# Kernel optimization log

Hardware: AMD Instinct MI355X
Metric: run time of the kernel (lower is better)

The kernel has to match this reference:

```python
import jax, jax.numpy as jnp
import numpy as np

N = 50000      # nodes
E = 800000     # edges (before self loops)
F_IN = 128     # dataset.num_features
HID = 32       # hidden_channels (per GAT head)
HEADS = 4
C = 40         # dataset.num_classes
NEG_SLOPE = 0.2


def setup_inputs() -> dict:
    key = jax.random.key(0)
    ks = jax.random.split(key, 18)
    g = lambda k, shape, fan: jax.random.normal(k, shape, dtype=jnp.float32) / np.sqrt(fan)
    inp = {
        "x": jax.random.normal(ks[0], (N, F_IN), dtype=jnp.float32),
        "edge_index": jax.random.randint(ks[1], (2, E), 0, N, dtype=jnp.int64),
        # GAT layer 1: F_IN -> HEADS*HID
        "gat_W1": g(ks[2], (F_IN, HEADS * HID), F_IN),
        "gat_att_src1": g(ks[3], (HEADS, HID), HID),
        "gat_att_dst1": g(ks[4], (HEADS, HID), HID),
        "gat_b1": jnp.zeros((HEADS * HID,), jnp.float32),
        # GAT layer 2: HEADS*HID -> C, heads=1
        "gat_W2": g(ks[5], (HEADS * HID, C), HEADS * HID),
        "gat_att_src2": g(ks[6], (1, C), C),
        "gat_att_dst2": g(ks[7], (1, C), C),
        "gat_b2": jnp.zeros((C,), jnp.float32),
        # GCN layers
        "gcn_W1": g(ks[8], (F_IN, HID), F_IN),
        "gcn_b1": jnp.zeros((HID,), jnp.float32),
        "gcn_W2": g(ks[9], (HID, C), HID),
        "gcn_b2": jnp.zeros((C,), jnp.float32),
        # final linear: 2C -> C
        "lin_W": g(ks[10], (2 * C, C), 2 * C),
        "lin_b": jnp.zeros((C,), jnp.float32),
        "weight_c": jnp.float32(0.5),
        "weight_t": jnp.float32(0.5),
    }
    return inp


def _add_self_loops(src, dst, n):
    loop = jnp.arange(n, dtype=src.dtype)
    return jnp.concatenate([src, loop]), jnp.concatenate([dst, loop])


def _gat_conv(x, src, dst, n, W, att_src, att_dst, b, heads, out_dim):
    # h: [n, heads, out_dim]
    h = (x @ W).reshape(n, heads, out_dim)
    a_s = jnp.einsum('nhd,hd->nh', h, att_src)   # source-side attention logit
    a_d = jnp.einsum('nhd,hd->nh', h, att_dst)   # target-side attention logit
    e = jax.nn.leaky_relu(a_s[src] + a_d[dst], NEG_SLOPE)  # [E', heads]
    # softmax over incoming edges of each target node (self loops guarantee >=1 edge)
    m = jax.ops.segment_max(e, dst, num_segments=n)
    ex = jnp.exp(e - m[dst])
    s = jax.ops.segment_sum(ex, dst, num_segments=n)
    alpha = ex / s[dst]                          # [E', heads]
    out = jax.ops.segment_sum(h[src] * alpha[..., None], dst, num_segments=n)
    return out.reshape(n, heads * out_dim) + b


def _gcn_conv(x, src, dst, n, W, b):
    h = x @ W
    deg = jax.ops.segment_sum(jnp.ones(src.shape, h.dtype), dst, num_segments=n)
    norm = jax.lax.rsqrt(deg)                    # deg >= 1 (self loops)
    coef = (norm[src] * norm[dst])[:, None]
    return jax.ops.segment_sum(h[src] * coef, dst, num_segments=n) + b


def reference(x, edge_index, gat_W1, gat_att_src1, gat_att_dst1, gat_b1,
              gat_W2, gat_att_src2, gat_att_dst2, gat_b2,
              gcn_W1, gcn_b1, gcn_W2, gcn_b2, lin_W, lin_b,
              weight_c, weight_t):
    n = x.shape[0]
    src, dst = _add_self_loops(edge_index[0], edge_index[1], n)
    # GAT branch (dropout is identity at inference)
    x_gat = _gat_conv(x, src, dst, n, gat_W1, gat_att_src1, gat_att_dst1,
                      gat_b1, HEADS, HID)
    x_gat = jax.nn.elu(x_gat)
    x_gat = _gat_conv(x_gat, src, dst, n, gat_W2, gat_att_src2, gat_att_dst2,
                      gat_b2, 1, C)
    # GCN branch
    x_gcn = jax.nn.relu(_gcn_conv(x, src, dst, n, gcn_W1, gcn_b1))
    x_gcn = _gcn_conv(x_gcn, src, dst, n, gcn_W2, gcn_b2)
    # weighted feature concat + linear head
    cat = jnp.concatenate([x_gcn * weight_c, x_gat * weight_t], axis=1)  # [n, 2C]
    return cat @ lin_W + lin_b
```

## Files before the change

kernel.cpp:

```cpp
#include <hip/hip_runtime.h>
#include <math.h>

#define F_IN   128
#define HIDC   32
#define NHEAD  4
#define CDIM   40
#define NEG_SLOPE 0.2f
#define BCAP   4096
#define OVCAP  16384
#define SCHUNK 4096

typedef __attribute__((ext_vector_type(8))) short bf16x8;
typedef __attribute__((ext_vector_type(4))) float f32x4;

__device__ __forceinline__ float leakyf(float x) { return x > 0.f ? x : NEG_SLOPE * x; }

__device__ __forceinline__ float wred_max(float v) {
#pragma unroll
    for (int o = 32; o > 0; o >>= 1) v = fmaxf(v, __shfl_xor(v, o, 64));
    return v;
}
__device__ __forceinline__ float wred_sum(float v) {
#pragma unroll
    for (int o = 32; o > 0; o >>= 1) v += __shfl_xor(v, o, 64);
    return v;
}
__device__ __forceinline__ float sel4(float4 v, int h) {
    return (h == 0) ? v.x : (h == 1) ? v.y : (h == 2) ? v.z : v.w;
}
__device__ __forceinline__ unsigned pack2_bf16(float a, float b) {
    unsigned ua = __float_as_uint(a);
    unsigned ub = __float_as_uint(b);
    ua = (ua + 0x7FFFu + ((ua >> 16) & 1u)) >> 16;
    ub = (ub + 0x7FFFu + ((ub >> 16) & 1u)) >> 16;
    return ua | (ub << 16);
}
__device__ __forceinline__ float2 unpack2_bf16(unsigned p) {
    return make_float2(__uint_as_float(p << 16), __uint_as_float(p & 0xFFFF0000u));
}

__global__ void wb_prep_kernel(const float* __restrict__ Wg, const float* __restrict__ Wc,
                               uint4* __restrict__ wbf)
{
    int b = blockIdx.x;
    int lane = threadIdx.x;
    int nt = b >> 2, ks = b & 3;
    int c = nt * 16 + (lane & 15);
    int k0 = ks * 32 + (lane >> 4) * 8;
    unsigned u[4];
#pragma unroll
    for (int jj = 0; jj < 4; ++jj) {
        int k = k0 + 2 * jj;
        float a0 = (c < 128) ? Wg[(size_t)k * 128 + c] : Wc[(size_t)k * 32 + (c - 128)];
        float a1 = (c < 128) ? Wg[(size_t)(k + 1) * 128 + c] : Wc[(size_t)(k + 1) * 32 + (c - 128)];
        u[jj] = pack2_bf16(a0, a1);
    }
    wbf[(size_t)b * 64 + lane] = make_uint4(u[0], u[1], u[2], u[3]);
}

__global__ __launch_bounds__(256) void gemm1_mfma_kernel(
    const float* __restrict__ X, const uint4* __restrict__ wbf,
    const float* __restrict__ aw_s, const float* __restrict__ aw_d,
    unsigned* __restrict__ h1b, unsigned* __restrict__ g1b,
    float* __restrict__ as1, float* __restrict__ ad1, int n)
{
    __shared__ float Ct[64][164];
    __shared__ float sw[128], dw[128];
    const int tid = threadIdx.x;
    const int w = tid >> 6, lane = tid & 63;
    const int m = lane & 15, q = lane >> 4;
    const int node0 = blockIdx.x * 64;
    if (tid < 128) { sw[tid] = aw_s[tid]; dw[tid] = aw_d[tid]; }

    f32x4 acc[10];
#pragma unroll
    for (int t = 0; t < 10; ++t) acc[t] = (f32x4){0.f, 0.f, 0.f, 0.f};

    const int row = node0 + w * 16 + m;
    const bool rv = row < n;
#pragma unroll
    for (int ks = 0; ks < 4; ++ks) {
        uint4 pa = make_uint4(0u, 0u, 0u, 0u);
        if (rv) {
            const float* xr = X + (size_t)row * 128 + ks * 32 + q * 8;
            float4 a0 = *(const float4*)xr;
            float4 a1 = *(const float4*)(xr + 4);
            pa = make_uint4(pack2_bf16(a0.x, a0.y), pack2_bf16(a0.z, a0.w),
                            pack2_bf16(a1.x, a1.y), pack2_bf16(a1.z, a1.w));
        }
        bf16x8 af = *(bf16x8*)&pa;
#pragma unroll
        for (int nt = 0; nt < 10; ++nt) {
            uint4 pb = wbf[(size_t)(nt * 4 + ks) * 64 + lane];
            bf16x8 bfv = *(bf16x8*)&pb;
            acc[nt] = __builtin_amdgcn_mfma_f32_16x16x32_bf16(af, bfv, acc[nt], 0, 0, 0);
        }
    }
#pragma unroll
    for (int nt = 0; nt < 10; ++nt)
#pragma unroll
        for (int r = 0; r < 4; ++r)
            Ct[w * 16 + q * 4 + r][nt * 16 + m] = acc[nt][r];
    __syncthreads();

    for (int i = tid; i < 64 * 64; i += 256) {
        int nd = i >> 6, u = i & 63;
        int gn = node0 + nd;
        if (gn < n)
            h1b[(size_t)gn * 64 + u] = pack2_bf16(Ct[nd][2 * u], Ct[nd][2 * u + 1]);
    }
    for (int i = tid; i < 64 * 16; i += 256) {
        int nd = i >> 4, u = i & 15;
        int gn = node0 + nd;
        if (gn < n)
            g1b[(size_t)gn * 16 + u] = pack2_bf16(Ct[nd][128 + 2 * u], Ct[nd][128 + 2 * u + 1]);
    }
    {
        int nd = tid >> 2, h = tid & 3;
        int gn = node0 + nd;
        if (gn < n) {
            float s = 0.f, d = 0.f;
#pragma unroll
            for (int k = 0; k < HIDC; ++k) {
                float v = Ct[nd][h * HIDC + k];
                s = fmaf(v, sw[h * HIDC + k], s);
                d = fmaf(v, dw[h * HIDC + k], d);
            }
            as1[(size_t)gn * 4 + h] = s;
            ad1[(size_t)gn * 4 + h] = d;
        }
    }
}

template<int K, int OUTC, int BN, int BK, int OSTRIDE = OUTC>
__global__ __launch_bounds__((OUTC / 4) * (BN / 4)) void gemm_tile(
    const float* __restrict__ X, const float* __restrict__ W,
    const float* __restrict__ bias, float* __restrict__ Y, int n)
{
    constexpr int CG = OUTC / 4;
    constexpr int NG = BN / 4;
    constexpr int NT = CG * NG;
    __shared__ float Xs[BK][BN + 4];
    __shared__ float Ws[BK][OUTC];
    const int tid = threadIdx.x;
    const int cg = tid % CG, ng = tid / CG;
    const int node0 = blockIdx.x * BN;
    float acc[4][4] = {};

    for (int kb = 0; kb < K; kb += BK) {
        for (int idx = tid; idx < BN * (BK / 4); idx += NT) {
            int nd = idx / (BK / 4);
            int kq = idx % (BK / 4);
            int gnode = node0 + nd;
            float4 v = (gnode < n) ? *(const float4*)&X[(size_t)gnode * K + kb + kq * 4]
                                   : make_float4(0.f, 0.f, 0.f, 0.f);
            Xs[kq * 4 + 0][nd] = v.x;
            Xs[kq * 4 + 1][nd] = v.y;
            Xs[kq * 4 + 2][nd] = v.z;
            Xs[kq * 4 + 3][nd] = v.w;
        }
        for (int idx = tid; idx < BK * CG; idx += NT) {
            int kk = idx / CG;
            int cq = idx % CG;
            *(float4*)&Ws[kk][cq * 4] = *(const float4*)&W[(size_t)(kb + kk) * OUTC + cq * 4];
        }
        __syncthreads();
#pragma unroll
        for (int k = 0; k < BK; ++k) {
            float4 xv = *(const float4*)&Xs[k][ng * 4];
            float4 wv = *(const float4*)&Ws[k][cg * 4];
            float xa[4] = {xv.x, xv.y, xv.z, xv.w};
            float wa[4] = {wv.x, wv.y, wv.z, wv.w};
#pragma unroll
            for (int j = 0; j < 4; ++j)
#pragma unroll
                for (int c = 0; c < 4; ++c)
                    acc[j][c] = fmaf(xa[j], wa[c], acc[j][c]);
        }
        __syncthreads();
    }

    float4 bv = make_float4(0.f, 0.f, 0.f, 0.f);
    if (bias) bv = *(const float4*)&bias[cg * 4];
#pragma unroll
    for (int j = 0; j < 4; ++j) {
        int gnode = node0 + ng * 4 + j;
        if (gnode < n) {
            float4 o = make_float4(acc[j][0] + bv.x, acc[j][1] + bv.y,
                                   acc[j][2] + bv.z, acc[j][3] + bv.w);
            *(float4*)&Y[(size_t)gnode * OSTRIDE + cg * 4] = o;
        }
    }
}

template<int K, int OUTC, int BN, int BK, int OSTRIDE_U, int OFF_U>
__global__ __launch_bounds__((OUTC / 4) * (BN / 4)) void gemm_tile_b(
    const float* __restrict__ X, const float* __restrict__ W,
    unsigned* __restrict__ Yb, int n)
{
    constexpr int CG = OUTC / 4;
    constexpr int NG = BN / 4;
    constexpr int NT = CG * NG;
    __shared__ float Xs[BK][BN + 4];
    __shared__ float Ws[BK][OUTC];
    const int tid = threadIdx.x;
    const int cg = tid % CG, ng = tid / CG;
    const int node0 = blockIdx.x * BN;
    float acc[4][4] = {};

    for (int kb = 0; kb < K; kb += BK) {
        for (int idx = tid; idx < BN * (BK / 4); idx += NT) {
            int nd = idx / (BK / 4);
            int kq = idx % (BK / 4);
            int gnode = node0 + nd;
            float4 v = (gnode < n) ? *(const float4*)&X[(size_t)gnode * K + kb + kq * 4]
                                   : make_float4(0.f, 0.f, 0.f, 0.f);
            Xs[kq * 4 + 0][nd] = v.x;
            Xs[kq * 4 + 1][nd] = v.y;
            Xs[kq * 4 + 2][nd] = v.z;
            Xs[kq * 4 + 3][nd] = v.w;
        }
        for (int idx = tid; idx < BK * CG; idx += NT) {
            int kk = idx / CG;
            int cq = idx % CG;
            *(float4*)&Ws[kk][cq * 4] = *(const float4*)&W[(size_t)(kb + kk) * OUTC + cq * 4];
        }
        __syncthreads();
#pragma unroll
        for (int k = 0; k < BK; ++k) {
            float4 xv = *(const float4*)&Xs[k][ng * 4];
            float4 wv = *(const float4*)&Ws[k][cg * 4];
            float xa[4] = {xv.x, xv.y, xv.z, xv.w};
            float wa[4] = {wv.x, wv.y, wv.z, wv.w};
#pragma unroll
            for (int j = 0; j < 4; ++j)
#pragma unroll
                for (int c = 0; c < 4; ++c)
                    acc[j][c] = fmaf(xa[j], wa[c], acc[j][c]);
        }
        __syncthreads();
    }

#pragma unroll
    for (int j = 0; j < 4; ++j) {
        int gnode = node0 + ng * 4 + j;
        if (gnode < n) {
            uint2 pb = make_uint2(pack2_bf16(acc[j][0], acc[j][1]),
                                  pack2_bf16(acc[j][2], acc[j][3]));
            *(uint2*)&Yb[(size_t)gnode * OSTRIDE_U + OFF_U + cg * 2] = pb;
        }
    }
}

template<int K, int OUTC, int BN, int BK, int OSTRIDE_U, int OFF_U>
__global__ __launch_bounds__((OUTC / 4) * (BN / 4)) void gemm_tile_bb(
    const unsigned* __restrict__ Xb, const float* __restrict__ W,
    unsigned* __restrict__ Yb, int n)
{
    constexpr int CG = OUTC / 4;
    constexpr int NG = BN / 4;
    constexpr int NT = CG * NG;
    __shared__ float Xs[BK][BN + 4];
    __shared__ float Ws[BK][OUTC];
    const int tid = threadIdx.x;
    const int cg = tid % CG, ng = tid / CG;
    const int node0 = blockIdx.x * BN;
    float acc[4][4] = {};

    for (int kb = 0; kb < K; kb += BK) {
        for (int idx = tid; idx < BN * (BK / 8); idx += NT) {
            int nd = idx / (BK / 8);
            int kq = idx % (BK / 8);
            int gnode = node0 + nd;
            uint4 v = (gnode < n) ? *(const uint4*)&Xb[(size_t)gnode * (K / 2) + kb / 2 + kq * 4]
                                  : make_uint4(0u, 0u, 0u, 0u);
            float2 a = unpack2_bf16(v.x), b = unpack2_bf16(v.y);
            float2 c = unpack2_bf16(v.z), d = unpack2_bf16(v.w);
            Xs[kq * 8 + 0][nd] = a.x; Xs[kq * 8 + 1][nd] = a.y;
            Xs[kq * 8 + 2][nd] = b.x; Xs[kq * 8 + 3][nd] = b.y;
            Xs[kq * 8 + 4][nd] = c.x; Xs[kq * 8 + 5][nd] = c.y;
            Xs[kq * 8 + 6][nd] = d.x; Xs[kq * 8 + 7][nd] = d.y;
        }
        for (int idx = tid; idx < BK * CG; idx += NT) {
            int kk = idx / CG;
            int cq = idx % CG;
            *(float4*)&Ws[kk][cq * 4] = *(const float4*)&W[(size_t)(kb + kk) * OUTC + cq * 4];
        }
        __syncthreads();
#pragma unroll
        for (int k = 0; k < BK; ++k) {
            float4 xv = *(const float4*)&Xs[k][ng * 4];
            float4 wv = *(const float4*)&Ws[k][cg * 4];
            float xa[4] = {xv.x, xv.y, xv.z, xv.w};
            float wa[4] = {wv.x, wv.y, wv.z, wv.w};
#pragma unroll
            for (int j = 0; j < 4; ++j)
#pragma unroll
                for (int c = 0; c < 4; ++c)
                    acc[j][c] = fmaf(xa[j], wa[c], acc[j][c]);
        }
        __syncthreads();
    }

#pragma unroll
    for (int j = 0; j < 4; ++j) {
        int gnode = node0 + ng * 4 + j;
        if (gnode < n) {
            uint2 pb = make_uint2(pack2_bf16(acc[j][0], acc[j][1]),
                                  pack2_bf16(acc[j][2], acc[j][3]));
            *(uint2*)&Yb[(size_t)gnode * OSTRIDE_U + OFF_U + cg * 2] = pb;
        }
    }
}

__global__ __launch_bounds__(256) void bucket_scatter_kernel(
    const int* __restrict__ src, const int* __restrict__ dst,
    unsigned* __restrict__ bcnt, unsigned* __restrict__ bpair,
    unsigned* __restrict__ ovf_cnt, uint2* __restrict__ ovf, int e, int nbuck)
{
    __shared__ unsigned hist[512];
    __shared__ unsigned base[512];
    const int t = threadIdx.x;
    const int lo = blockIdx.x * SCHUNK;
    const int hi = min(lo + SCHUNK, e);
    for (int i = t; i < nbuck; i += 256) hist[i] = 0;
    __syncthreads();
    for (int i = lo + t; i < hi; i += 256)
        atomicAdd(&hist[((unsigned)dst[i]) >> 7], 1u);
    __syncthreads();
    for (int i = t; i < nbuck; i += 256) {
        unsigned c = hist[i];
        base[i] = c ? atomicAdd(&bcnt[i], c) : 0u;
        hist[i] = 0;
    }
    __syncthreads();
    for (int i = lo + t; i < hi; i += 256) {
        unsigned s = (unsigned)src[i], d = (unsigned)dst[i];
        unsigned b = d >> 7;
        unsigned pos = base[b] + atomicAdd(&hist[b], 1u);
        if (pos < BCAP) bpair[(size_t)b * BCAP + pos] = s | ((d & 127u) << 16);
        else {
            unsigned o = atomicAdd(ovf_cnt, 1u);
            if (o < OVCAP) ovf[o] = make_uint2(s, d);
        }
    }
}

__global__ __launch_bounds__(256) void bucket_count_kernel(
    const unsigned* __restrict__ bcnt, const unsigned* __restrict__ bpair,
    const unsigned* __restrict__ ovf_cnt, const uint2* __restrict__ ovf,
    unsigned* __restrict__ counts, int n)
{
    __shared__ unsigned lc[128];
    const int b = blockIdx.x, base = b << 7;
    if (threadIdx.x < 128) lc[threadIdx.x] = 0;
    __syncthreads();
    unsigned bc = bcnt[b];
    int cnt = (int)(bc < BCAP ? bc : BCAP);
    for (int k = threadIdx.x; k < cnt; k += 256)
        atomicAdd(&lc[bpair[(size_t)b * BCAP + k] >> 16], 1u);
    unsigned oc_u = *ovf_cnt;
    int oc = (int)(oc_u < OVCAP ? oc_u : OVCAP);
    for (int k = threadIdx.x; k < oc; k += 256) {
        uint2 pp = ovf[k];
        if ((int)(pp.y >> 7) == b) atomicAdd(&lc[pp.y & 127u], 1u);
    }
    __syncthreads();
    int i = base + threadIdx.x;
    if (threadIdx.x < 128 && i < n) counts[i] = lc[threadIdx.x];
}

__global__ __launch_bounds__(256) void scan_reduce_kernel(const unsigned* __restrict__ counts,
                                                          unsigned* __restrict__ partials, int n)
{
    __shared__ unsigned sm[256];
    int t = threadIdx.x;
    int i = blockIdx.x * 256 + t;
    unsigned v = (i < n) ? counts[i] : 0u;
    sm[t] = v;
    __syncthreads();
#pragma unroll
    for (int off = 128; off > 0; off >>= 1) {
        if (t < off) sm[t] += sm[t + off];
        __syncthreads();
    }
    if (t == 0) partials[blockIdx.x] = sm[0];
}

__global__ __launch_bounds__(256) void scan_partials_kernel(unsigned* __restrict__ partials,
                                                            unsigned* __restrict__ rs, int nb, int n)
{
    __shared__ unsigned sm[256];
    int t = threadIdx.x;
    unsigned v = (t < nb) ? partials[t] : 0u;
    sm[t] = v;
    __syncthreads();
#pragma unroll
    for (int off = 1; off < 256; off <<= 1) {
        unsigned u = (t >= off) ? sm[t - off] : 0u;
        __syncthreads();
        sm[t] += u;
        __syncthreads();
    }
    if (t < nb) partials[t] = sm[t] - v;
    if (t == 255) rs[n] = sm[255];
}

__global__ __launch_bounds__(256) void scan_write_kernel(const unsigned* __restrict__ counts,
                                                         const unsigned* __restrict__ partials,
                                                         unsigned* __restrict__ rs,
                                                         float* __restrict__ nrm, int n)
{
    __shared__ unsigned sm[256];
    int t = threadIdx.x;
    int i = blockIdx.x * 256 + t;
    unsigned c = (i < n) ? counts[i] : 0u;
    sm[t] = c;
    __syncthreads();
#pragma unroll
    for (int off = 1; off < 256; off <<= 1) {
        unsigned u = (t >= off) ? sm[t - off] : 0u;
        __syncthreads();
        sm[t] += u;
        __syncthreads();
    }
    if (i < n) {
        rs[i] = partials[blockIdx.x] + sm[t] - c;
        nrm[i] = rsqrtf((float)(c + 1u));
    }
}

__global__ __launch_bounds__(256) void bucket_place_kernel(
    const unsigned* __restrict__ bcnt, const unsigned* __restrict__ bpair,
    const unsigned* __restrict__ rs, unsigned* __restrict__ csr_src,
    unsigned* __restrict__ cursor, int n)
{
    __shared__ unsigned lc[128];
    __shared__ unsigned rbase[128];
    const int b = blockIdx.x, base = b << 7;
    if (threadIdx.x < 128) {
        lc[threadIdx.x] = 0;
        int i = base + threadIdx.x;
        rbase[threadIdx.x] = (i < n) ? rs[i] : 0u;
    }
    __syncthreads();
    unsigned bc = bcnt[b];
    int cnt = (int)(bc < BCAP ? bc : BCAP);
    for (int k = threadIdx.x; k < cnt; k += 256) {
        unsigned v = bpair[(size_t)b * BCAP + k];
        unsigned ld = v >> 16;
        unsigned r = atomicAdd(&lc[ld], 1u);
        csr_src[rbase[ld] + r] = v & 0xFFFFu;
    }
    __syncthreads();
    int i = base + threadIdx.x;
    if (threadIdx.x < 128 && i < n) cursor[i] = rbase[threadIdx.x] + lc[threadIdx.x];
}

__global__ void overflow_fill_kernel(const unsigned* __restrict__ ovf_cnt,
                                     const uint2* __restrict__ ovf,
                                     unsigned* __restrict__ cursor,
                                     unsigned* __restrict__ csr_src)
{
    unsigned oc_u = *ovf_cnt;
    int oc = (int)(oc_u < OVCAP ? oc_u : OVCAP);
    for (int k = threadIdx.x; k < oc; k += 256) {
        uint2 pp = ovf[k];
        unsigned pos = atomicAdd(&cursor[pp.y], 1u);
        csr_src[pos] = pp.x;
    }
}

__global__ void logits2_kernel(const unsigned* __restrict__ hg_b, const float* __restrict__ aw_s,
                               const float* __restrict__ aw_d, float* __restrict__ as2,
                               float* __restrict__ ad2, int n)
{
    __shared__ float sw[CDIM], dw[CDIM];
    if (threadIdx.x < CDIM) { sw[threadIdx.x] = aw_s[threadIdx.x]; dw[threadIdx.x] = aw_d[threadIdx.x]; }
    __syncthreads();
    int i = blockIdx.x * 256 + threadIdx.x;
    if (i >= n) return;
    const unsigned* row = hg_b + (size_t)i * 40;
    float s = 0.f, d = 0.f;
#pragma unroll
    for (int k = 0; k < 20; ++k) {
        float2 v = unpack2_bf16(row[k]);
        s = fmaf(v.x, sw[2 * k], s);     s = fmaf(v.y, sw[2 * k + 1], s);
        d = fmaf(v.x, dw[2 * k], d);     d = fmaf(v.y, dw[2 * k + 1], d);
    }
    as2[i] = s; ad2[i] = d;
}

#define CAP1 96
__global__ __launch_bounds__(256) void gat_agg1_kernel(
    const unsigned* __restrict__ h1b,
    const float* __restrict__ as1, const float* __restrict__ ad1,
    const unsigned* __restrict__ rs, const unsigned* __restrict__ csr_src,
    const float* __restrict__ b1, unsigned* __restrict__ xgb, int n)
{
    __shared__ unsigned sidx[4][CAP1];
    __shared__ float    w4[4][CAP1][4];
    const int wid = threadIdx.x >> 6;
    const int lane = threadIdx.x & 63;
    const int i = blockIdx.x * 4 + wid;
    if (i >= n) return;
    const unsigned beg = rs[i];
    const int deg = (int)(rs[i + 1] - beg);
    const float4* as1v = (const float4*)as1;
    float4 av = as1v[i];
    float4 dv = ((const float4*)ad1)[i];
    float4 es = make_float4(leakyf(av.x + dv.x), leakyf(av.y + dv.y),
                            leakyf(av.z + dv.z), leakyf(av.w + dv.w));
    float m0 = es.x, m1 = es.y, m2 = es.z, m3 = es.w;
    for (int k = lane; k < deg; k += 64) {
        unsigned s = csr_src[beg + k];
        float4 a = as1v[s];
        float e0 = leakyf(a.x + dv.x), e1 = leakyf(a.y + dv.y);
        float e2 = leakyf(a.z + dv.z), e3 = leakyf(a.w + dv.w);
        if (k < CAP1) {
            sidx[wid][k] = s;
            w4[wid][k][0] = e0; w4[wid][k][1] = e1;
            w4[wid][k][2] = e2; w4[wid][k][3] = e3;
        }
        m0 = fmaxf(m0, e0); m1 = fmaxf(m1, e1);
        m2 = fmaxf(m2, e2); m3 = fmaxf(m3, e3);
    }
    m0 = wred_max(m0); m1 = wred_max(m1); m2 = wred_max(m2); m3 = wred_max(m3);
    float s0 = 0.f, s1 = 0.f, s2 = 0.f, s3 = 0.f;
    if (lane == 0) {
        s0 = __expf(es.x - m0); s1 = __expf(es.y - m1);
        s2 = __expf(es.z - m2); s3 = __expf(es.w - m3);
    }
    const int dc = deg < CAP1 ? deg : CAP1;
    for (int k = lane; k < dc; k += 64) {
        float w0 = __expf(w4[wid][k][0] - m0); w4[wid][k][0] = w0; s0 += w0;
        float w1 = __expf(w4[wid][k][1] - m1); w4[wid][k][1] = w1; s1 += w1;
        float w2 = __expf(w4[wid][k][2] - m2); w4[wid][k][2] = w2; s2 += w2;
        float w3 = __expf(w4[wid][k][3] - m3); w4[wid][k][3] = w3; s3 += w3;
    }
    for (int k = CAP1 + lane; k < deg; k += 64) {
        unsigned s = csr_src[beg + k];
        float4 a = as1v[s];
        s0 += __expf(leakyf(a.x + dv.x) - m0);
        s1 += __expf(leakyf(a.y + dv.y) - m1);
        s2 += __expf(leakyf(a.z + dv.z) - m2);
        s3 += __expf(leakyf(a.w + dv.w) - m3);
    }
    s0 = wred_sum(s0); s1 = wred_sum(s1); s2 = wred_sum(s2); s3 = wred_sum(s3);
    __threadfence_block();
    const int h = lane >> 4;
    const float mh   = sel4(make_float4(m0, m1, m2, m3), h);
    const float advh = sel4(dv, h);
    const float ssh  = sel4(make_float4(s0, s1, s2, s3), h);
    const float wself = __expf(sel4(es, h) - mh);
    float2 hv = unpack2_bf16(h1b[(size_t)i * 64 + lane]);
    float2 acc = make_float2(hv.x * wself, hv.y * wself);
    auto edge = [&](int j, unsigned& s, float& w) {
        if (j < CAP1) { s = sidx[wid][j]; w = w4[wid][j][h]; }
        else {
            s = csr_src[beg + j];
            float4 a = as1v[s];
            w = __expf(leakyf(sel4(a, h) + advh) - mh);
        }
    };
    int j = 0;
    for (; j + 4 <= deg; j += 4) {
        unsigned sa, sb, sc, sd; float wa, wb, wc, wd;
        edge(j, sa, wa); edge(j + 1, sb, wb); edge(j + 2, sc, wc); edge(j + 3, sd, wd);
        float2 va = unpack2_bf16(h1b[(size_t)sa * 64 + lane]);
        float2 vb = unpack2_bf16(h1b[(size_t)sb * 64 + lane]);
        float2 vc = unpack2_bf16(h1b[(size_t)sc * 64 + lane]);
        float2 vd = unpack2_bf16(h1b[(size_t)sd * 64 + lane]);
        acc.x = fmaf(va.x, wa, acc.x); acc.y = fmaf(va.y, wa, acc.y);
        acc.x = fmaf(vb.x, wb, acc.x); acc.y = fmaf(vb.y, wb, acc.y);
        acc.x = fmaf(vc.x, wc, acc.x); acc.y = fmaf(vc.y, wc, acc.y);
        acc.x = fmaf(vd.x, wd, acc.x); acc.y = fmaf(vd.y, wd, acc.y);
    }
    for (; j < deg; ++j) {
        unsigned s; float w; edge(j, s, w);
        float2 v = unpack2_bf16(h1b[(size_t)s * 64 + lane]);
        acc.x = fmaf(v.x, w, acc.x); acc.y = fmaf(v.y, w, acc.y);
    }
    float inv = 1.f / ssh;
    int c0 = 2 * lane;
    float o0 = acc.x * inv + b1[c0];
    float o1 = acc.y * inv + b1[c0 + 1];
    o0 = o0 > 0.f ? o0 : __expf(o0) - 1.f;
    o1 = o1 > 0.f ? o1 : __expf(o1) - 1.f;
    xgb[(size_t)i * 64 + lane] = pack2_bf16(o0, o1);
}

#define CAP2 128
__global__ __launch_bounds__(256) void agg2_fused_kernel(
    const unsigned* __restrict__ hg_b, const float* __restrict__ as2,
    const float* __restrict__ ad2, const float* __restrict__ nrm,
    const unsigned* __restrict__ rs, const unsigned* __restrict__ csr_src,
    const float* __restrict__ gat_b2, const float* __restrict__ gcn_b2,
    const float* __restrict__ wc_p, const float* __restrict__ wt_p,
    float* __restrict__ cat, int n)
{
    __shared__ unsigned sidx[4][CAP2];
    __shared__ float    wgt[4][CAP2];
    __shared__ float    cf [4][CAP2];
    const int wid = threadIdx.x >> 6;
    const int lane = threadIdx.x & 63;
    const int i = blockIdx.x * 4 + wid;
    if (i >= n) return;
    const unsigned beg = rs[i];
    const int deg = (int)(rs[i + 1] - beg);
    const float adv = ad2[i];
    const float e_self = leakyf(as2[i] + adv);
    const float ni = nrm[i];
    float m = e_self;
    for (int k = lane; k < deg; k += 64) {
        unsigned s = csr_src[beg + k];
        float e = leakyf(as2[s] + adv);
        if (k < CAP2) { sidx[wid][k] = s; wgt[wid][k] = e; cf[wid][k] = nrm[s]; }
        m = fmaxf(m, e);
    }
    m = wred_max(m);
    float ssum = (lane == 0) ? __expf(e_self - m) : 0.f;
    const int dc = deg < CAP2 ? deg : CAP2;
    for (int k = lane; k < dc; k += 64) {
        float w = __expf(wgt[wid][k] - m);
        wgt[wid][k] = w; ssum += w;
    }
    for (int k = CAP2 + lane; k < deg; k += 64) {
        unsigned s = csr_src[beg + k];
        ssum += __expf(leakyf(as2[s] + adv) - m);
    }
    ssum = wred_sum(ssum);
    __threadfence_block();
    const bool act   = lane < 40;
    const bool isgat = lane < 20;
    const float selfw = isgat ? __expf(e_self - m) : ni * ni;
    float2 acc = make_float2(0.f, 0.f);
    if (act) {
        float2 v = unpack2_bf16(hg_b[(size_t)i * 40 + lane]);
        acc.x = v.x * selfw; acc.y = v.y * selfw;
    }
    auto edge = [&](int j, unsigned& s, float& w) {
        if (j < CAP2) {
            s = sidx[wid][j];
            w = isgat ? wgt[wid][j] : cf[wid][j] * ni;
        } else {
            s = csr_src[beg + j];
            w = isgat ? __expf(leakyf(as2[s] + adv) - m) : nrm[s] * ni;
        }
    };
    int j = 0;
    for (; j + 4 <= deg; j += 4) {
        unsigned sa, sb, sc, sd; float wa, wb, wc, wd;
        edge(j, sa, wa); edge(j + 1, sb, wb); edge(j + 2, sc, wc); edge(j + 3, sd, wd);
        if (act) {
            float2 va = unpack2_bf16(hg_b[(size_t)sa * 40 + lane]);
            float2 vb = unpack2_bf16(hg_b[(size_t)sb * 40 + lane]);
            float2 vc = unpack2_bf16(hg_b[(size_t)sc * 40 + lane]);
            float2 vd = unpack2_bf16(hg_b[(size_t)sd * 40 + lane]);
            acc.x = fmaf(va.x, wa, acc.x); acc.y = fmaf(va.y, wa, acc.y);
            acc.x = fmaf(vb.x, wb, acc.x); acc.y = fmaf(vb.y, wb, acc.y);
            acc.x = fmaf(vc.x, wc, acc.x); acc.y = fmaf(vc.y, wc, acc.y);
            acc.x = fmaf(vd.x, wd, acc.x); acc.y = fmaf(vd.y, wd, acc.y);
        }
    }
    for (; j < deg; ++j) {
        unsigned s; float w; edge(j, s, w);
        if (act) {
            float2 v = unpack2_bf16(hg_b[(size_t)s * 40 + lane]);
            acc.x = fmaf(v.x, w, acc.x); acc.y = fmaf(v.y, w, acc.y);
        }
    }
    if (act) {
        if (isgat) {
            float inv = 1.f / ssum, wt = *wt_p;
            int c0 = 2 * lane;
            cat[(size_t)i * 80 + 40 + c0]     = (acc.x * inv + gat_b2[c0]) * wt;
            cat[(size_t)i * 80 + 40 + c0 + 1] = (acc.y * inv + gat_b2[c0 + 1]) * wt;
        } else {
            float wc = *wc_p;
            int c0 = 2 * (lane - 20);
            cat[(size_t)i * 80 + c0]     = (acc.x + gcn_b2[c0]) * wc;
            cat[(size_t)i * 80 + c0 + 1] = (acc.y + gcn_b2[c0 + 1]) * wc;
        }
    }
}

#define CAPG 128
__global__ __launch_bounds__(256) void gcn_agg1_kernel(
    const unsigned short* __restrict__ g1b, const float* __restrict__ nrm,
    const unsigned* __restrict__ rs, const unsigned* __restrict__ csr_src,
    const float* __restrict__ b, float* __restrict__ out, int n)
{
    __shared__ unsigned sidx[4][CAPG];
    __shared__ float    cf[4][CAPG];
    const int wid = threadIdx.x >> 6;
    const int lane = threadIdx.x & 63;
    const int i = blockIdx.x * 4 + wid;
    if (i >= n) return;
    const unsigned beg = rs[i];
    const int deg = (int)(rs[i + 1] - beg);
    const float ni = nrm[i];
    const int dcg = deg < CAPG ? deg : CAPG;
    for (int k = lane; k < dcg; k += 64) {
        unsigned s = csr_src[beg + k];
        sidx[wid][k] = s; cf[wid][k] = nrm[s];
    }
    __threadfence_block();
    const int half = lane >> 5, c = lane & 31;
    auto ldb = [&](unsigned node) {
        return __uint_as_float(((unsigned)g1b[(size_t)node * 32 + c]) << 16);
    };
    float acc = (half == 0) ? ldb(i) * ni * ni : 0.f;
    auto edge = [&](int j, unsigned& s, float& w) {
        if (j < CAPG) { s = sidx[wid][j]; w = cf[wid][j] * ni; }
        else { s = csr_src[beg + j]; w = nrm[s] * ni; }
    };
    int j = half;
    for (; j + 2 < deg; j += 4) {
        unsigned sa, sb; float wa, wb;
        edge(j, sa, wa); edge(j + 2, sb, wb);
        float va = ldb(sa);
        float vb = ldb(sb);
        acc = fmaf(va, wa, acc);
        acc = fmaf(vb, wb, acc);
    }
    for (; j < deg; j += 2) {
        unsigned s; float w; edge(j, s, w);
        acc = fmaf(ldb(s), w, acc);
    }
    acc += __shfl_xor(acc, 32, 64);
    if (half == 0) out[(size_t)i * 32 + c] = fmaxf(acc + b[c], 0.f);
}

extern "C" void kernel_launch(void* const* d_in, const int* in_sizes, int n_in,
                              void* d_out, int out_size, void* d_ws, size_t ws_size,
                              hipStream_t stream)
{
    const float* x        = (const float*)d_in[0];
    const int*   eidx     = (const int*)d_in[1];
    const float* gat_W1   = (const float*)d_in[2];
    const float* att_s1   = (const float*)d_in[3];
    const float* att_d1   = (const float*)d_in[4];
    const float* gat_b1   = (const float*)d_in[5];
    const float* gat_W2   = (const float*)d_in[6];
    const float* att_s2   = (const float*)d_in[7];
    const float* att_d2   = (const float*)d_in[8];
    const float* gat_b2   = (const float*)d_in[9];
    const float* gcn_W1   = (const float*)d_in[10];
    const float* gcn_b1   = (const float*)d_in[11];
    const float* gcn_W2   = (const float*)d_in[12];
    const float* gcn_b2   = (const float*)d_in[13];
    const float* lin_W    = (const float*)d_in[14];
    const float* lin_b    = (const float*)d_in[15];
    const float* wc_p     = (const float*)d_in[16];
    const float* wt_p     = (const float*)d_in[17];

    const int n = in_sizes[0] / F_IN;
    const int e = in_sizes[1] / 2;
    const int* src = eidx;
    const int* dst = eidx + e;
    const int NBUCK = (n + 127) >> 7;

    char* p = (char*)d_ws;
    auto alloc = [&](size_t bytes) -> void* {
        void* r = (void*)p;
        p += (bytes + 255) & ~(size_t)255;
        return r;
    };
    unsigned* counts  = (unsigned*)alloc((size_t)n * 4);
    unsigned* rs      = (unsigned*)alloc((size_t)(n + 1) * 4);
    unsigned* cursor  = (unsigned*)alloc((size_t)n * 4);
    unsigned* partials= (unsigned*)alloc(256 * 4);
    unsigned* bcnt    = (unsigned*)alloc((size_t)(NBUCK + 1) * 4);
    unsigned* csr_src = (unsigned*)alloc((size_t)e * 4);
    uint4*    wbf     = (uint4*)alloc(40 * 64 * 16);
    float* nrm     = (float*)alloc((size_t)n * 4);
    float* as1     = (float*)alloc((size_t)n * 4 * 4);
    float* ad1     = (float*)alloc((size_t)n * 4 * 4);
    float* as2     = (float*)alloc((size_t)n * 4);
    float* ad2     = (float*)alloc((size_t)n * 4);
    float* cat     = (float*)alloc((size_t)n * 80 * 4);
    unsigned* hg_b = (unsigned*)alloc((size_t)n * 40 * 4);
    float* xg      = (float*)alloc((size_t)n * F_IN * 4);
    unsigned* g1b  = (unsigned*)alloc((size_t)n * 16 * 4);
    unsigned* bpair = (unsigned*)cat;
    uint2*    ovf   = (uint2*)(bpair + (size_t)NBUCK * BCAP);
    unsigned* h1b   = (unsigned*)cat;
    float*    gacc1 = xg;
    unsigned* xgb   = (unsigned*)xg;
    unsigned* ovf_cnt = bcnt + NBUCK;

    const int NB = (n + 255) / 256;
    const int WB = (n + 3) / 4;
    const int SB = (e + SCHUNK - 1) / SCHUNK;

    hipMemsetAsync(bcnt, 0, (size_t)(NBUCK + 1) * 4, stream);
    bucket_scatter_kernel<<<SB, 256, 0, stream>>>(src, dst, bcnt, bpair, ovf_cnt, ovf, e, NBUCK);
    bucket_count_kernel<<<NBUCK, 256, 0, stream>>>(bcnt, bpair, ovf_cnt, ovf, counts, n);
    scan_reduce_kernel<<<NB, 256, 0, stream>>>(counts, partials, n);
    scan_partials_kernel<<<1, 256, 0, stream>>>(partials, rs, NB, n);
    scan_write_kernel<<<NB, 256, 0, stream>>>(counts, partials, rs, nrm, n);
    bucket_place_kernel<<<NBUCK, 256, 0, stream>>>(bcnt, bpair, rs, csr_src, cursor, n);
    overflow_fill_kernel<<<1, 256, 0, stream>>>(ovf_cnt, ovf, cursor, csr_src);

    wb_prep_kernel<<<40, 64, 0, stream>>>(gat_W1, gcn_W1, wbf);
    gemm1_mfma_kernel<<<(n + 63) / 64, 256, 0, stream>>>(x, wbf, att_s1, att_d1,
                                                         h1b, g1b, as1, ad1, n);

    gcn_agg1_kernel<<<WB, 256, 0, stream>>>((const unsigned short*)g1b, nrm, rs, csr_src,
                                            gcn_b1, gacc1, n);
    gemm_tile_b<32, 40, 128, 32, 40, 20><<<(n + 127) / 128, 320, 0, stream>>>(gacc1, gcn_W2, hg_b, n);

    gat_agg1_kernel<<<WB, 256, 0, stream>>>(h1b, as1, ad1, rs, csr_src, gat_b1, xgb, n);
    gemm_tile_bb<128, 40, 128, 32, 40, 0><<<(n + 127) / 128, 320, 0, stream>>>(xgb, gat_W2, hg_b, n);
    logits2_kernel<<<NB, 256, 0, stream>>>(hg_b, att_s2, att_d2, as2, ad2, n);

    agg2_fused_kernel<<<WB, 256, 0, stream>>>(hg_b, as2, ad2, nrm, rs, csr_src,
                                              gat_b2, gcn_b2, wc_p, wt_p, cat, n);

    gemm_tile<80, 40, 128, 40><<<(n + 127) / 128, 320, 0, stream>>>(cat, lin_W, lin_b, (float*)d_out, n);
}
```

Baseline: 340.3 us.

## Fuse GCN layer-1 aggregation into GAT layer-1 aggregation kernel

Merges the separate GCN first-layer aggregation into the GAT first-layer aggregation kernel. Both walk the same CSR neighbor lists, so the indices and normalisation coefficients are loaded once and the GCN accumulation runs on the first 32 lanes alongside the GAT gather. The GCN hidden output is now stored as bf16 and fed to the bf16-input GEMM, which halves that intermediate's traffic. The cost is extra per-edge loads and registers in the fused kernel, possible lane divergence, and lower precision for the GCN hidden features.

```diff
diff --git a/kernel.cpp b/kernel.cpp
--- a/kernel.cpp
+++ b/kernel.cpp
@@ -37,6 +37,9 @@
 }
 __device__ __forceinline__ float2 unpack2_bf16(unsigned p) {
     return make_float2(__uint_as_float(p << 16), __uint_as_float(p & 0xFFFF0000u));
+}
+__device__ __forceinline__ float bf2f(unsigned short u) {
+    return __uint_as_float(((unsigned)u) << 16);
 }
 
 __global__ void wb_prep_kernel(const float* __restrict__ Wg, const float* __restrict__ Wc,
@@ -189,65 +192,6 @@
             float4 o = make_float4(acc[j][0] + bv.x, acc[j][1] + bv.y,
                                    acc[j][2] + bv.z, acc[j][3] + bv.w);
             *(float4*)&Y[(size_t)gnode * OSTRIDE + cg * 4] = o;
-        }
-    }
-}
-
-template<int K, int OUTC, int BN, int BK, int OSTRIDE_U, int OFF_U>
-__global__ __launch_bounds__((OUTC / 4) * (BN / 4)) void gemm_tile_b(
-    const float* __restrict__ X, const float* __restrict__ W,
-    unsigned* __restrict__ Yb, int n)
-{
-    constexpr int CG = OUTC / 4;
-    constexpr int NG = BN / 4;
-    constexpr int NT = CG * NG;
-    __shared__ float Xs[BK][BN + 4];
-    __shared__ float Ws[BK][OUTC];
-    const int tid = threadIdx.x;
-    const int cg = tid % CG, ng = tid / CG;
-    const int node0 = blockIdx.x * BN;
-    float acc[4][4] = {};
-
-    for (int kb = 0; kb < K; kb += BK) {
-        for (int idx = tid; idx < BN * (BK / 4); idx += NT) {
-            int nd = idx / (BK / 4);
-            int kq = idx % (BK / 4);
-            int gnode = node0 + nd;
-            float4 v = (gnode < n) ? *(const float4*)&X[(size_t)gnode * K + kb + kq * 4]
-                                   : make_float4(0.f, 0.f, 0.f, 0.f);
-            Xs[kq * 4 + 0][nd] = v.x;
-            Xs[kq * 4 + 1][nd] = v.y;
-            Xs[kq * 4 + 2][nd] = v.z;
-            Xs[kq * 4 + 3][nd] = v.w;
-        }
-        for (int idx = tid; idx < BK * CG; idx += NT) {
-            int kk = idx / CG;
-            int cq = idx % CG;
-            *(float4*)&Ws[kk][cq * 4] = *(const float4*)&W[(size_t)(kb + kk) * OUTC + cq * 4];
-        }
-        __syncthreads();
-#pragma unroll
-        for (int k = 0; k < BK; ++k) {
-            float4 xv = *(const float4*)&Xs[k][ng * 4];
-            float4 wv = *(const float4*)&Ws[k][cg * 4];
-            float xa[4] = {xv.x, xv.y, xv.z, xv.w};
-            float wa[4] = {wv.x, wv.y, wv.z, wv.w};
-#pragma unroll
-            for (int j = 0; j < 4; ++j)
-#pragma unroll
-                for (int c = 0; c < 4; ++c)
-                    acc[j][c] = fmaf(xa[j], wa[c], acc[j][c]);
-        }
-        __syncthreads();
-    }
-
-#pragma unroll
-    for (int j = 0; j < 4; ++j) {
-        int gnode = node0 + ng * 4 + j;
-        if (gnode < n) {
-            uint2 pb = make_uint2(pack2_bf16(acc[j][0], acc[j][1]),
-                                  pack2_bf16(acc[j][2], acc[j][3]));
-            *(uint2*)&Yb[(size_t)gnode * OSTRIDE_U + OFF_U + cg * 2] = pb;
         }
     }
 }
@@ -492,14 +436,17 @@
 }
 
 #define CAP1 96
-__global__ __launch_bounds__(256) void gat_agg1_kernel(
-    const unsigned* __restrict__ h1b,
+__global__ __launch_bounds__(256) void agg1_fused_kernel(
+    const unsigned* __restrict__ h1b, const unsigned short* __restrict__ g1b,
     const float* __restrict__ as1, const float* __restrict__ ad1,
+    const float* __restrict__ nrm,
     const unsigned* __restrict__ rs, const unsigned* __restrict__ csr_src,
-    const float* __restrict__ b1, unsigned* __restrict__ xgb, int n)
+    const float* __restrict__ gat_b1, const float* __restrict__ gcn_b1,
+    unsigned* __restrict__ xgb, unsigned* __restrict__ gaccb, int n)
 {
     __shared__ unsigned sidx[4][CAP1];
     __shared__ float    w4[4][CAP1][4];
+    __shared__ float    cf[4][CAP1];
     const int wid = threadIdx.x >> 6;
     const int lane = threadIdx.x & 63;
     const int i = blockIdx.x * 4 + wid;
@@ -509,6 +456,7 @@
     const float4* as1v = (const float4*)as1;
     float4 av = as1v[i];
     float4 dv = ((const float4*)ad1)[i];
+    const float ni = nrm[i];
     float4 es = make_float4(leakyf(av.x + dv.x), leakyf(av.y + dv.y),
                             leakyf(av.z + dv.z), leakyf(av.w + dv.w));
     float m0 = es.x, m1 = es.y, m2 = es.z, m3 = es.w;
@@ -521,6 +469,7 @@
             sidx[wid][k] = s;
             w4[wid][k][0] = e0; w4[wid][k][1] = e1;
             w4[wid][k][2] = e2; w4[wid][k][3] = e3;
+            cf[wid][k] = nrm[s];
         }
         m0 = fmaxf(m0, e0); m1 = fmaxf(m1, e1);
         m2 = fmaxf(m2, e2); m3 = fmaxf(m3, e3);
@@ -553,41 +502,58 @@
     const float advh = sel4(dv, h);
     const float ssh  = sel4(make_float4(s0, s1, s2, s3), h);
     const float wself = __expf(sel4(es, h) - mh);
+    const bool gact = lane < 32;
     float2 hv = unpack2_bf16(h1b[(size_t)i * 64 + lane]);
     float2 acc = make_float2(hv.x * wself, hv.y * wself);
-    auto edge = [&](int j, unsigned& s, float& w) {
-        if (j < CAP1) { s = sidx[wid][j]; w = w4[wid][j][h]; }
+    float gacc = gact ? bf2f(g1b[(size_t)i * 32 + lane]) * ni * ni : 0.f;
+    auto edge = [&](int j, unsigned& s, float& w, float& c) {
+        if (j < CAP1) { s = sidx[wid][j]; w = w4[wid][j][h]; c = cf[wid][j]; }
         else {
             s = csr_src[beg + j];
             float4 a = as1v[s];
             w = __expf(leakyf(sel4(a, h) + advh) - mh);
+            c = nrm[s];
         }
     };
     int j = 0;
     for (; j + 4 <= deg; j += 4) {
-        unsigned sa, sb, sc, sd; float wa, wb, wc, wd;
-        edge(j, sa, wa); edge(j + 1, sb, wb); edge(j + 2, sc, wc); edge(j + 3, sd, wd);
-        float2 va = unpack2_bf16(h1b[(size_t)sa * 64 + lane]);
-        float2 vb = unpack2_bf16(h1b[(size_t)sb * 64 + lane]);
-        float2 vc = unpack2_bf16(h1b[(size_t)sc * 64 + lane]);
-        float2 vd = unpack2_bf16(h1b[(size_t)sd * 64 + lane]);
-        acc.x = fmaf(va.x, wa, acc.x); acc.y = fmaf(va.y, wa, acc.y);
-        acc.x = fmaf(vb.x, wb, acc.x); acc.y = fmaf(vb.y, wb, acc.y);
-        acc.x = fmaf(vc.x, wc, acc.x); acc.y = fmaf(vc.y, wc, acc.y);
-        acc.x = fmaf(vd.x, wd, acc.x); acc.y = fmaf(vd.y, wd, acc.y);
+        unsigned ss[4]; float ww[4], cc[4];
+#pragma unroll
+        for (int t = 0; t < 4; ++t) edge(j + t, ss[t], ww[t], cc[t]);
+        unsigned pv[4];
+#pragma unroll
+        for (int t = 0; t < 4; ++t) pv[t] = h1b[(size_t)ss[t] * 64 + lane];
+        float gv[4];
+        if (gact) {
+#pragma unroll
+            for (int t = 0; t < 4; ++t) gv[t] = bf2f(g1b[(size_t)ss[t] * 32 + lane]);
+        }
+#pragma unroll
+        for (int t = 0; t < 4; ++t) {
+            float2 v = unpack2_bf16(pv[t]);
+            acc.x = fmaf(v.x, ww[t], acc.x);
+            acc.y = fmaf(v.y, ww[t], acc.y);
+            if (gact) gacc = fmaf(gv[t], cc[t] * ni, gacc);
+        }
     }
     for (; j < deg; ++j) {
-        unsigned s; float w; edge(j, s, w);
+        unsigned s; float w, c; edge(j, s, w, c);
         float2 v = unpack2_bf16(h1b[(size_t)s * 64 + lane]);
-        acc.x = fmaf(v.x, w, acc.x); acc.y = fmaf(v.y, w, acc.y);
+        acc.x = fmaf(v.x, w, acc.x);
+        acc.y = fmaf(v.y, w, acc.y);
+        if (gact) gacc = fmaf(bf2f(g1b[(size_t)s * 32 + lane]), c * ni, gacc);
     }
     float inv = 1.f / ssh;
     int c0 = 2 * lane;
-    float o0 = acc.x * inv + b1[c0];
-    float o1 = acc.y * inv + b1[c0 + 1];
+    float o0 = acc.x * inv + gat_b1[c0];
+    float o1 = acc.y * inv + gat_b1[c0 + 1];
     o0 = o0 > 0.f ? o0 : __expf(o0) - 1.f;
     o1 = o1 > 0.f ? o1 : __expf(o1) - 1.f;
     xgb[(size_t)i * 64 + lane] = pack2_bf16(o0, o1);
+    float go = gact ? fmaxf(gacc + gcn_b1[lane], 0.f) : 0.f;
+    float gp = __shfl_xor(go, 1, 64);
+    if (gact && (lane & 1) == 0)
+        gaccb[(size_t)i * 16 + (lane >> 1)] = pack2_bf16(go, gp);
 }
 
 #define CAP2 128
@@ -683,53 +649,6 @@
             cat[(size_t)i * 80 + c0 + 1] = (acc.y + gcn_b2[c0 + 1]) * wc;
         }
     }
-}
-
-#define CAPG 128
-__global__ __launch_bounds__(256) void gcn_agg1_kernel(
-    const unsigned short* __restrict__ g1b, const float* __restrict__ nrm,
-    const unsigned* __restrict__ rs, const unsigned* __restrict__ csr_src,
-    const float* __restrict__ b, float* __restrict__ out, int n)
-{
-    __shared__ unsigned sidx[4][CAPG];
-    __shared__ float    cf[4][CAPG];
-    const int wid = threadIdx.x >> 6;
-    const int lane = threadIdx.x & 63;
-    const int i = blockIdx.x * 4 + wid;
-    if (i >= n) return;
-    const unsigned beg = rs[i];
-    const int deg = (int)(rs[i + 1] - beg);
-    const float ni = nrm[i];
-    const int dcg = deg < CAPG ? deg : CAPG;
-    for (int k = lane; k < dcg; k += 64) {
-        unsigned s = csr_src[beg + k];
-        sidx[wid][k] = s; cf[wid][k] = nrm[s];
-    }
-    __threadfence_block();
-    const int half = lane >> 5, c = lane & 31;
-    auto ldb = [&](unsigned node) {
-        return __uint_as_float(((unsigned)g1b[(size_t)node * 32 + c]) << 16);
-    };
-    float acc = (half == 0) ? ldb(i) * ni * ni : 0.f;
-    auto edge = [&](int j, unsigned& s, float& w) {
-        if (j < CAPG) { s = sidx[wid][j]; w = cf[wid][j] * ni; }
-        else { s = csr_src[beg + j]; w = nrm[s] * ni; }
-    };
-    int j = half;
-    for (; j + 2 < deg; j += 4) {
-        unsigned sa, sb; float wa, wb;
-        edge(j, sa, wa); edge(j + 2, sb, wb);
-        float va = ldb(sa);
-        float vb = ldb(sb);
-        acc = fmaf(va, wa, acc);
-        acc = fmaf(vb, wb, acc);
-    }
-    for (; j < deg; j += 2) {
-        unsigned s; float w; edge(j, s, w);
-        acc = fmaf(ldb(s), w, acc);
-    }
-    acc += __shfl_xor(acc, 32, 64);
-    if (half == 0) out[(size_t)i * 32 + c] = fmaxf(acc + b[c], 0.f);
 }
 
 extern "C" void kernel_launch(void* const* d_in, const int* in_sizes, int n_in,
@@ -783,10 +702,10 @@
     unsigned* hg_b = (unsigned*)alloc((size_t)n * 40 * 4);
     float* xg      = (float*)alloc((size_t)n * F_IN * 4);
     unsigned* g1b  = (unsigned*)alloc((size_t)n * 16 * 4);
+    unsigned* gaccb= (unsigned*)alloc((size_t)n * 16 * 4);
     unsigned* bpair = (unsigned*)cat;
     uint2*    ovf   = (uint2*)(bpair + (size_t)NBUCK * BCAP);
     unsigned* h1b   = (unsigned*)cat;
-    float*    gacc1 = xg;
     unsigned* xgb   = (unsigned*)xg;
     unsigned* ovf_cnt = bcnt + NBUCK;
 
@@ -807,11 +726,11 @@
     gemm1_mfma_kernel<<<(n + 63) / 64, 256, 0, stream>>>(x, wbf, att_s1, att_d1,
                                                          h1b, g1b, as1, ad1, n);
 
-    gcn_agg1_kernel<<<WB, 256, 0, stream>>>((const unsigned short*)g1b, nrm, rs, csr_src,
-                                            gcn_b1, gacc1, n);
-    gemm_tile_b<32, 40, 128, 32, 40, 20><<<(n + 127) / 128, 320, 0, stream>>>(gacc1, gcn_W2, hg_b, n);
-
-    gat_agg1_kernel<<<WB, 256, 0, stream>>>(h1b, as1, ad1, rs, csr_src, gat_b1, xgb, n);
+    agg1_fused_kernel<<<WB, 256, 0, stream>>>(h1b, (const unsigned short*)g1b,
+                                              as1, ad1, nrm, rs, csr_src,
+                                              gat_b1, gcn_b1, xgb, gaccb, n);
+
+    gemm_tile_bb<32, 40, 128, 32, 40, 20><<<(n + 127) / 128, 320, 0, stream>>>(gaccb, gcn_W2, hg_b, n);
     gemm_tile_bb<128, 40, 128, 32, 40, 0><<<(n + 127) / 128, 320, 0, stream>>>(xgb, gat_W2, hg_b, n);
     logits2_kernel<<<NB, 256, 0, stream>>>(hg_b, att_s2, att_d2, as2, ad2, n);
 
```

Measured after the change: 323.7 us. -4.9%, faster.
